# Optimization experiments

Measured on AMD Instinct MI355X. Metric: run time of the kernel, lower is better.

## Reference

```python
import jax, jax.numpy as jnp
import numpy as np

B, C, H, W = 2, 3, 512, 512
P = 16
D = 768
NH = 12
DEPTH = 12
MLP = 4
HP, WP = H // P, W // P
N = HP * WP
DH = D // NH          # 64
ROPE_BASE = 100.0     # from pos_embed='RoPE100'


def _ln(x, w, b, eps):
    m = jnp.mean(x, -1, keepdims=True)
    v = jnp.mean((x - m) ** 2, -1, keepdims=True)
    return (x - m) * jax.lax.rsqrt(v + eps) * w + b


def _rope_tables(maxpos, d):
    inv = 1.0 / (ROPE_BASE ** (jnp.arange(0, d, 2, dtype=jnp.float32) / d))
    f = jnp.arange(maxpos, dtype=jnp.float32)[:, None] * inv[None, :]
    f = jnp.concatenate([f, f], -1)  # [maxpos, d]
    return jnp.cos(f), jnp.sin(f)


def _rot_half(x):
    x1, x2 = jnp.split(x, 2, -1)
    return jnp.concatenate([-x2, x1], -1)


def _rope2d(t, pos, cos, sin):
    # t: [B,NH,N,DH]; pos: [B,N,2] (y,x). First half of DH rotated by y, second by x.
    def rot1d(tok, p):
        c = cos[p][:, None]  # [B,1,N,DH//2]
        s = sin[p][:, None]
        return tok * c + _rot_half(tok) * s
    ty, tx = jnp.split(t, 2, -1)
    return jnp.concatenate([rot1d(ty, pos[..., 0]), rot1d(tx, pos[..., 1])], -1)


def _forward(image, patch_w, patch_b, ln1_w, ln1_b, qkv_w, qkv_b, proj_w, proj_b,
             ln2_w, ln2_b, fc1_w, fc1_b, fc2_w, fc2_b, encn_w, encn_b):
    # patch embed: conv stride=patch, flatten row-major (y-major, matching cartesian_prod(y,x))
    x = jax.lax.conv_general_dilated(image, patch_w, (P, P), 'VALID',
                                     dimension_numbers=('NCHW', 'OIHW', 'NCHW'))
    x = (x + patch_b[None, :, None, None]).reshape(B, D, N).transpose(0, 2, 1)  # [B,N,D]
    yy, xx = jnp.meshgrid(jnp.arange(HP), jnp.arange(WP), indexing='ij')
    pos = jnp.broadcast_to(jnp.stack([yy, xx], -1).reshape(N, 2), (B, N, 2))
    cos, sin = _rope_tables(max(HP, WP), DH // 2)
    scale = DH ** -0.5
    for i in range(DEPTH):
        h = _ln(x, ln1_w[i], ln1_b[i], 1e-5)
        qkv = (h @ qkv_w[i].T + qkv_b[i]).reshape(B, N, 3, NH, DH).transpose(2, 0, 3, 1, 4)
        q, k, v = qkv[0], qkv[1], qkv[2]  # [B,NH,N,DH]
        q = _rope2d(q, pos, cos, sin)
        k = _rope2d(k, pos, cos, sin)
        att = jax.nn.softmax(jnp.einsum('bhqd,bhkd->bhqk', q, k) * scale, -1)
        o = jnp.einsum('bhqk,bhkd->bhqd', att, v).transpose(0, 2, 1, 3).reshape(B, N, D)
        x = x + o @ proj_w[i].T + proj_b[i]
        h = _ln(x, ln2_w[i], ln2_b[i], 1e-5)
        h = jax.nn.gelu(h @ fc1_w[i].T + fc1_b[i], approximate=False)
        x = x + h @ fc2_w[i].T + fc2_b[i]
    x = _ln(x, encn_w, encn_b, 1e-6)
    return x, pos


def setup_inputs() -> dict:
    key = jax.random.key(0)
    ks = jax.random.split(key, 8)
    s = 0.02
    dff = MLP * D
    return {
        "image": jax.random.normal(ks[0], (B, C, H, W), jnp.float32),
        "true_shape": jnp.full((B, 2), H, jnp.int32),
        "patch_w": jax.random.normal(ks[1], (D, C, P, P), jnp.float32) * s,
        "patch_b": jnp.zeros((D,), jnp.float32),
        "ln1_w": jnp.ones((DEPTH, D), jnp.float32),
        "ln1_b": jnp.zeros((DEPTH, D), jnp.float32),
        "qkv_w": jax.random.normal(ks[2], (DEPTH, 3 * D, D), jnp.float32) * s,
        "qkv_b": jnp.zeros((DEPTH, 3 * D), jnp.float32),
        "proj_w": jax.random.normal(ks[3], (DEPTH, D, D), jnp.float32) * s,
        "proj_b": jnp.zeros((DEPTH, D), jnp.float32),
        "ln2_w": jnp.ones((DEPTH, D), jnp.float32),
        "ln2_b": jnp.zeros((DEPTH, D), jnp.float32),
        "fc1_w": jax.random.normal(ks[4], (DEPTH, dff, D), jnp.float32) * s,
        "fc1_b": jnp.zeros((DEPTH, dff), jnp.float32),
        "fc2_w": jax.random.normal(ks[5], (DEPTH, D, dff), jnp.float32) * s,
        "fc2_b": jnp.zeros((DEPTH, D), jnp.float32),
        "encn_w": jnp.ones((D,), jnp.float32),
        "encn_b": jnp.zeros((D,), jnp.float32),
    }


def reference(image, true_shape, patch_w, patch_b, ln1_w, ln1_b, qkv_w, qkv_b,
              proj_w, proj_b, ln2_w, ln2_b, fc1_w, fc1_b, fc2_w, fc2_b,
              encn_w, encn_b):
    # true_shape assumed full-resolution (all images H x W); positions are static grid
    return _forward(image, patch_w, patch_b, ln1_w, ln1_b, qkv_w, qkv_b, proj_w,
                    proj_b, ln2_w, ln2_b, fc1_w, fc1_b, fc2_w, fc2_b, encn_w, encn_b)
```

## Files before the change

kernel.cpp:

```cpp
#include <hip/hip_runtime.h>
#include <hip/hip_bf16.h>
#include <stdint.h>

typedef unsigned short u16;
typedef __attribute__((ext_vector_type(8))) short bf16x8;
typedef __attribute__((ext_vector_type(4))) float f32x4;
typedef __attribute__((ext_vector_type(4))) u16 u16x4;
typedef __attribute__((ext_vector_type(4))) uint32_t u32x4;

__device__ __forceinline__ u16 f2bf(float f) {
  union { float f; uint32_t u; } v; v.f = f;
  uint32_t u = v.u + 0x7FFFu + ((v.u >> 16) & 1u);
  return (u16)(u >> 16);
}
__device__ __forceinline__ float bf2f(u16 h) {
  union { uint32_t u; float f; } v; v.u = ((uint32_t)h) << 16;
  return v.f;
}

__device__ __forceinline__ int xcd_swz(int hw, int n) {
  return (n & 7) ? hw : (hw & 7) * (n >> 3) + (hw >> 3);
}

__device__ __forceinline__ void gload_lds16(const void* g, void* l) {
  __builtin_amdgcn_global_load_lds(
      (const __attribute__((address_space(1))) void*)g,
      (__attribute__((address_space(3))) void*)l, 16, 0, 0);
}

__global__ __launch_bounds__(256) void cast_f32_bf16(const float* __restrict__ src,
                                                     u16* __restrict__ dst, int n4) {
  int i = blockIdx.x * 256 + threadIdx.x;
  if (i < n4) {
    float4 v = ((const float4*)src)[i];
    u16x4 o; o.x = f2bf(v.x); o.y = f2bf(v.y); o.z = f2bf(v.z); o.w = f2bf(v.w);
    ((u16x4*)dst)[i] = o;
  }
}

__global__ __launch_bounds__(256) void im2col_kernel(const float* __restrict__ img,
                                                     u16* __restrict__ out) {
  int f = blockIdx.x * 256 + threadIdx.x;
  int row = blockIdx.y;
  int b = row >> 10, n = row & 1023, py = n >> 5, px = n & 31;
  int c = f >> 8, rem = f & 255, i = rem >> 4, j = rem & 15;
  float v = img[(((size_t)b * 3 + c) * 512 + py * 16 + i) * 512 + px * 16 + j];
  out[(size_t)row * 768 + f] = f2bf(v);
}

template <int EPI>
__global__ __launch_bounds__(256, 2)
void gemm_bt(const u16* __restrict__ A, const u16* __restrict__ W,
             const float* __restrict__ bias, void* __restrict__ outp,
             int M, int N, int K, int lda, int ldw) {
  constexpr int AB = 128 * 128;
  constexpr int BB = 128 * 128;
  constexpr int BUF = AB + BB;
  constexpr int LOADS = BUF / 4096;
  __shared__ char smem[2 * BUF];
  const int tid = threadIdx.x;
  const int lane = tid & 63;
  const int w = tid >> 6;
  const int qr = lane & 15;
  const int kg = lane >> 4;
  const int gx = gridDim.x;
  const int lid = xcd_swz(blockIdx.x + blockIdx.y * gx, gx * gridDim.y);
  const int bn = lid % gx, bm = lid / gx;
  const int wr = (w >> 1) * 64;
  const int wc = (w & 1) * 64;
  const size_t arow0 = (size_t)bm * 128;
  const size_t wrow0 = (size_t)bn * 128;
  const u16* Ab = A + (size_t)blockIdx.z * K;
  const u16* Wb = W + (size_t)blockIdx.z * K;

  f32x4 acc[4][4] = {};

  auto stage = [&](int buf, int kt) {
    char* As = smem + buf * BUF;
    char* Ws = As + AB;
#pragma unroll
    for (int r = 0; r < 4; ++r) {
      int o = r * 4096 + tid * 16;
      int row = o >> 7;
      int lc = (o & 127) ^ ((row & 7) << 4);
      gload_lds16(Ab + (arow0 + row) * lda + kt + (lc >> 1), As + o);
    }
#pragma unroll
    for (int r = 0; r < 4; ++r) {
      int o = r * 4096 + tid * 16;
      int row = o >> 7;
      int lc = (o & 127) ^ ((row & 7) << 4);
      gload_lds16(Wb + (wrow0 + row) * ldw + kt + (lc >> 1), Ws + o);
    }
  };

  const int nt = K >> 6;
  stage(0, 0);
  stage(1, 64);
  for (int t = 0; t < nt; ++t) {
    if (t + 1 < nt) {
      asm volatile("s_waitcnt vmcnt(%0)" :: "i"(LOADS) : "memory");
    } else {
      asm volatile("s_waitcnt vmcnt(0)" ::: "memory");
    }
    __builtin_amdgcn_s_barrier();
    const char* As = smem + (t & 1) * BUF;
    const char* Ws = As + AB;
    bf16x8 af[2][4], bfr[2][4];
#pragma unroll
    for (int m = 0; m < 4; ++m) {
      int row = wr + m * 16 + qr;
      af[0][m] = *(const bf16x8*)(As + row * 128 + ((kg * 16) ^ ((row & 7) << 4)));
    }
#pragma unroll
    for (int n = 0; n < 4; ++n) {
      int row = wc + n * 16 + qr;
      bfr[0][n] = *(const bf16x8*)(Ws + row * 128 + ((kg * 16) ^ ((row & 7) << 4)));
    }
    __builtin_amdgcn_sched_barrier(0);
#pragma unroll
    for (int m = 0; m < 4; ++m) {
      int row = wr + m * 16 + qr;
      af[1][m] = *(const bf16x8*)(As + row * 128 + ((64 + kg * 16) ^ ((row & 7) << 4)));
    }
#pragma unroll
    for (int n = 0; n < 4; ++n) {
      int row = wc + n * 16 + qr;
      bfr[1][n] = *(const bf16x8*)(Ws + row * 128 + ((64 + kg * 16) ^ ((row & 7) << 4)));
    }
    asm volatile("s_waitcnt lgkmcnt(8)" ::: "memory");
    __builtin_amdgcn_sched_barrier(0);
#pragma unroll
    for (int m = 0; m < 4; ++m)
#pragma unroll
      for (int n = 0; n < 4; ++n)
        acc[m][n] = __builtin_amdgcn_mfma_f32_16x16x32_bf16(af[0][m], bfr[0][n], acc[m][n], 0, 0, 0);
    asm volatile("s_waitcnt lgkmcnt(0)" ::: "memory");
    __builtin_amdgcn_sched_barrier(0);
    __builtin_amdgcn_s_barrier();
    if (t + 2 < nt) stage(t & 1, (t + 2) << 6);
#pragma unroll
    for (int m = 0; m < 4; ++m)
#pragma unroll
      for (int n = 0; n < 4; ++n)
        acc[m][n] = __builtin_amdgcn_mfma_f32_16x16x32_bf16(af[1][m], bfr[1][n], acc[m][n], 0, 0, 0);
  }

  const int r0 = bm * 128 + wr + kg * 4;
  const int c0 = bn * 128 + wc + qr;
  if constexpr (EPI == 4) {
    const int headbase = bn * 128 + wc;
    const bool isqk = headbase < 1536;
    const float linv = exp2f(-0.41524101186092122f * (float)qr);
    u16* outb = (u16*)outp;
#pragma unroll
    for (int m = 0; m < 4; ++m) {
#pragma unroll
      for (int j = 0; j < 4; ++j) {
        int row = r0 + m * 16 + j;
        int tok = row & 1023;
        float vs[4];
#pragma unroll
        for (int n = 0; n < 4; ++n) vs[n] = acc[m][n][j] + bias[c0 + n * 16];
        if (isqk) {
          float sy, cy, sx, cx;
          __sincosf((float)(tok >> 5) * linv, &sy, &cy);
          __sincosf((float)(tok & 31) * linv, &sx, &cx);
          float a0 = vs[0], a1 = vs[1], a2 = vs[2], a3 = vs[3];
          vs[0] = a0 * cy - a1 * sy;
          vs[1] = a1 * cy + a0 * sy;
          vs[2] = a2 * cx - a3 * sx;
          vs[3] = a3 * cx + a2 * sx;
        }
#pragma unroll
        for (int n = 0; n < 4; ++n)
          outb[(size_t)row * N + c0 + n * 16] = f2bf(vs[n]);
      }
    }
  } else if constexpr (EPI == 5) {
    u16* outb = (u16*)outp + (size_t)blockIdx.z * M * N;
#pragma unroll
    for (int m = 0; m < 4; ++m)
#pragma unroll
      for (int j = 0; j < 4; ++j) {
        int row = r0 + m * 16 + j;
#pragma unroll
        for (int n = 0; n < 4; ++n)
          outb[(size_t)row * N + c0 + n * 16] = f2bf(acc[m][n][j]);
      }
  } else {
    u16* outb = (u16*)outp;
#pragma unroll
    for (int m = 0; m < 4; ++m)
#pragma unroll
      for (int j = 0; j < 4; ++j) {
        int row = r0 + m * 16 + j;
#pragma unroll
        for (int n = 0; n < 4; ++n) {
          int col = c0 + n * 16;
          float v = acc[m][n][j] + bias[col];
          v = 0.5f * v * (1.0f + erff(v * 0.70710678118654752f));
          outb[(size_t)row * N + col] = f2bf(v);
        }
      }
  }
}

template <int FINAL>
__global__ __launch_bounds__(192)
void fuse_red_ln(const u16* __restrict__ parts, const float* __restrict__ bias,
                 const float* __restrict__ resid, float* __restrict__ xout,
                 void* __restrict__ lnout, const float* __restrict__ lw,
                 const float* __restrict__ lb, float eps) {
  if (FINAL && blockIdx.x >= 2048) {
    int i = (blockIdx.x - 2048) * 192 + threadIdx.x;
    if (i < 4096) {
      int c = i & 1, n = (i >> 1) & 1023;
      ((float*)lnout)[(size_t)2048 * 768 + i] = (float)(c ? (n & 31) : (n >> 5));
    }
    return;
  }
  const int row = blockIdx.x, t = threadIdx.x;
  const int c0 = t * 4;
  constexpr size_t MN = (size_t)2048 * 768;
  const u16x4 pa = *(const u16x4*)(parts + (size_t)row * 768 + c0);
  const u16x4 pb = *(const u16x4*)(parts + MN + (size_t)row * 768 + c0);
  const f32x4 bi = *(const f32x4*)(bias + c0);
  f32x4 v;
#pragma unroll
  for (int j = 0; j < 4; ++j) v[j] = bf2f(pa[j]) + bf2f(pb[j]) + bi[j];
  if (resid) v += *(const f32x4*)(resid + (size_t)row * 768 + c0);
  *(f32x4*)(xout + (size_t)row * 768 + c0) = v;
  float s = (v[0] + v[1]) + (v[2] + v[3]);
  float sq = (v[0] * v[0] + v[1] * v[1]) + (v[2] * v[2] + v[3] * v[3]);
#pragma unroll
  for (int m = 1; m < 64; m <<= 1) {
    s += __shfl_xor(s, m);
    sq += __shfl_xor(sq, m);
  }
  __shared__ float red[6];
  int wv = t >> 6;
  if ((t & 63) == 0) { red[wv] = s; red[3 + wv] = sq; }
  __syncthreads();
  s = red[0] + red[1] + red[2];
  sq = red[3] + red[4] + red[5];
  float mean = s * (1.0f / 768.0f);
  float var = sq * (1.0f / 768.0f) - mean * mean;
  float rstd = rsqrtf(var + eps);
  const f32x4 lwv = *(const f32x4*)(lw + c0);
  const f32x4 lbv = *(const f32x4*)(lb + c0);
  if (FINAL) {
    f32x4 o;
#pragma unroll
    for (int j = 0; j < 4; ++j) o[j] = (v[j] - mean) * rstd * lwv[j] + lbv[j];
    *(f32x4*)((float*)lnout + (size_t)row * 768 + c0) = o;
  } else {
    u16x4 o;
#pragma unroll
    for (int j = 0; j < 4; ++j) o[j] = f2bf((v[j] - mean) * rstd * lwv[j] + lbv[j]);
    *(u16x4*)((u16*)lnout + (size_t)row * 768 + c0) = o;
  }
}

__global__ __launch_bounds__(256)
void attn_kernel(const u16* __restrict__ qkv, u16* __restrict__ o) {
  __shared__ char smem[32768];
  const int tid = threadIdx.x, lane = tid & 63, w = tid >> 6;
  const int qr = lane & 15, kg = lane >> 4;
  const bool kgodd = (kg & 1) != 0;
  const int lid = xcd_swz(blockIdx.x, gridDim.x);
  const int qb = lid & 15, bh = lid >> 4;
  const int b = bh / 12, h = bh % 12;
  const int qrow0 = qb * 64 + w * 16;
  const u16* kvb = qkv + (size_t)b * 1024 * 2304;

  bf16x8 aq[2];
  {
    const u16* qbase = qkv + ((size_t)(b * 1024 + qrow0 + qr)) * 2304 + h * 64;
    aq[0] = *(const bf16x8*)(qbase + kg * 8);
    aq[1] = *(const bf16x8*)(qbase + 32 + kg * 8);
#pragma unroll
    for (int r = 0; r < 2; ++r)
#pragma unroll
      for (int e = 0; e < 8; ++e)
        aq[r][e] = (short)f2bf(bf2f((u16)aq[r][e]) * 0.125f);
  }
  f32x4 oacc[4] = {};
  float lsum = 0.f;

  const int kvp = tid >> 3, dg = tid & 7;
  bf16x8 va, vb;
  auto issueV = [&](int kt) {
    const u16* vsrc = kvb + ((size_t)(kt * 64 + kvp * 2)) * 2304 + 1536 + h * 64 + dg * 8;
    va = *(const bf16x8*)vsrc;
    vb = *(const bf16x8*)(vsrc + 2304);
  };
  auto issueK = [&](int kt, int bsel) {
    char* Ks = smem + bsel * 8192;
#pragma unroll
    for (int r = 0; r < 2; ++r) {
      int off = r * 4096 + tid * 16;
      int kv = off >> 7;
      int db = (off ^ ((kv & 7) << 4)) & 127;
      gload_lds16(kvb + ((size_t)(kt * 64 + kv)) * 2304 + 768 + h * 64 + (db >> 1), Ks + off);
    }
  };
  auto writeV = [&](int bsel) {
    char* Vt = smem + 16384 + bsel * 8192;
#pragma unroll
    for (int j = 0; j < 8; ++j) {
      int d = dg * 8 + j;
      uint32_t pk = (uint32_t)(u16)va[j] | ((uint32_t)(u16)vb[j] << 16);
      *(uint32_t*)(Vt + ((d * 128 + kvp * 4) ^ (((dg ^ j) & 7) << 4))) = pk;
    }
  };

  issueV(0);
  issueK(0, 0);
  writeV(0);

  for (int kt = 0; kt < 16; ++kt) {
    const int c = kt & 1;
    asm volatile("s_waitcnt vmcnt(0) lgkmcnt(0)" ::: "memory");
    __builtin_amdgcn_s_barrier();
    if (kt + 1 < 16) { issueV(kt + 1); issueK(kt + 1, c ^ 1); }

    const char* Ks = smem + c * 8192;
    const char* Vt = smem + 16384 + c * 8192;

    bf16x8 bk[2][4];
#pragma unroll
    for (int n = 0; n < 4; ++n) {
      int row = n * 16 + qr;
      bk[0][n] = *(const bf16x8*)(Ks + ((row * 128 + kg * 16) ^ ((row & 7) << 4)));
    }
    __builtin_amdgcn_sched_barrier(0);
#pragma unroll
    for (int n = 0; n < 4; ++n) {
      int row = n * 16 + qr;
      bk[1][n] = *(const bf16x8*)(Ks + ((row * 128 + 64 + kg * 16) ^ ((row & 7) << 4)));
    }
    f32x4 sa[4] = {};
    asm volatile("s_waitcnt lgkmcnt(4)" ::: "memory");
    __builtin_amdgcn_sched_barrier(0);
    __builtin_amdgcn_s_setprio(1);
#pragma unroll
    for (int n = 0; n < 4; ++n)
      sa[n] = __builtin_amdgcn_mfma_f32_16x16x32_bf16(bk[0][n], aq[0], sa[n], 0, 0, 0);
    asm volatile("s_waitcnt lgkmcnt(0)" ::: "memory");
    __builtin_amdgcn_sched_barrier(0);
#pragma unroll
    for (int n = 0; n < 4; ++n)
      sa[n] = __builtin_amdgcn_mfma_f32_16x16x32_bf16(bk[1][n], aq[1], sa[n], 0, 0, 0);
    __builtin_amdgcn_s_setprio(0);

    float pv[4][4];
    float ts = 0.f;
#pragma unroll
    for (int n = 0; n < 4; ++n)
#pragma unroll
      for (int j = 0; j < 4; ++j) {
        pv[n][j] = __expf(sa[n][j]);
        ts += pv[n][j];
      }
    lsum += ts;

    if (kt + 1 < 16) writeV(c ^ 1);

    bf16x8 vf[2][4];
#pragma unroll
    for (int ks = 0; ks < 2; ++ks)
#pragma unroll
      for (int n = 0; n < 4; ++n) {
        int d = n * 16 + qr;
        vf[ks][n] = *(const bf16x8*)(Vt + ((d * 128 + ks * 64 + kg * 16) ^ ((((d >> 3) ^ (d & 7)) & 7) << 4)));
      }

    uint32_t pk0[4], pk1[4];
#pragma unroll
    for (int n = 0; n < 4; ++n) {
      asm("v_cvt_pk_bf16_f32 %0, %1, %2" : "=v"(pk0[n]) : "v"(pv[n][0]), "v"(pv[n][1]));
      asm("v_cvt_pk_bf16_f32 %0, %1, %2" : "=v"(pk1[n]) : "v"(pv[n][2]), "v"(pv[n][3]));
    }
    bf16x8 pb[2];
#pragma unroll
    for (int ks = 0; ks < 2; ++ks) {
      uint32_t A0 = pk0[ks * 2], B0 = pk0[ks * 2 + 1];
      uint32_t A1 = pk1[ks * 2], B1 = pk1[ks * 2 + 1];
      asm("v_permlane32_swap_b32 %0, %1" : "+v"(A0), "+v"(B0));
      asm("v_permlane32_swap_b32 %0, %1" : "+v"(A1), "+v"(B1));
      uint32_t sA0 = (uint32_t)__shfl_xor((int)A0, 16);
      uint32_t sA1 = (uint32_t)__shfl_xor((int)A1, 16);
      uint32_t sB0 = (uint32_t)__shfl_xor((int)B0, 16);
      uint32_t sB1 = (uint32_t)__shfl_xor((int)B1, 16);
      u32x4 dd;
      dd.x = kgodd ? sB0 : A0;
      dd.y = kgodd ? sB1 : A1;
      dd.z = kgodd ? B0 : sA0;
      dd.w = kgodd ? B1 : sA1;
      pb[ks] = __builtin_bit_cast(bf16x8, dd);
    }

    __builtin_amdgcn_s_setprio(1);
#pragma unroll
    for (int ks = 0; ks < 2; ++ks)
#pragma unroll
      for (int n = 0; n < 4; ++n)
        oacc[n] = __builtin_amdgcn_mfma_f32_16x16x32_bf16(vf[ks][n], pb[ks], oacc[n], 0, 0, 0);
    __builtin_amdgcn_s_setprio(0);
  }
  lsum += __shfl_xor(lsum, 16);
  lsum += __shfl_xor(lsum, 32);
  float inv = 1.0f / lsum;
  const size_t rowg = (size_t)(b * 1024 + qrow0 + qr);
#pragma unroll
  for (int n = 0; n < 4; ++n) {
    u16x4 ov;
#pragma unroll
    for (int j = 0; j < 4; ++j) ov[j] = f2bf(oacc[n][j] * inv);
    *(u16x4*)(o + rowg * 768 + h * 64 + n * 16 + kg * 4) = ov;
  }
}

extern "C" void kernel_launch(void* const* d_in, const int* in_sizes, int n_in,
                              void* d_out, int out_size, void* d_ws, size_t ws_size,
                              hipStream_t stream) {
  const float* image  = (const float*)d_in[0];
  const float* patch_w = (const float*)d_in[2];
  const float* patch_b = (const float*)d_in[3];
  const float* ln1_w = (const float*)d_in[4];
  const float* ln1_b = (const float*)d_in[5];
  const float* qkv_w = (const float*)d_in[6];
  const float* qkv_b = (const float*)d_in[7];
  const float* proj_w = (const float*)d_in[8];
  const float* proj_b = (const float*)d_in[9];
  const float* ln2_w = (const float*)d_in[10];
  const float* ln2_b = (const float*)d_in[11];
  const float* fc1_w = (const float*)d_in[12];
  const float* fc1_b = (const float*)d_in[13];
  const float* fc2_w = (const float*)d_in[14];
  const float* fc2_b = (const float*)d_in[15];
  const float* encn_w = (const float*)d_in[16];
  const float* encn_b = (const float*)d_in[17];

  char* ws = (char*)d_ws;
  size_t off = 0;
  auto alloc = [&](size_t bytes) {
    char* pr = ws + off;
    off += (bytes + 255) & ~(size_t)255;
    return pr;
  };

  float* x    = (float*)alloc((size_t)2048 * 768 * 4);
  u16* hbuf   = (u16*)alloc((size_t)2048 * 768 * 2);
  u16* qkvb   = (u16*)alloc((size_t)2048 * 2304 * 2);
  u16* obuf   = (u16*)alloc((size_t)2048 * 768 * 2);
  u16* h2     = (u16*)alloc((size_t)2048 * 3072 * 2);
  u16* wpb    = (u16*)alloc((size_t)768 * 768 * 2);
  u16* parts  = (u16*)alloc((size_t)2 * 2048 * 768 * 2);

  const size_t wq_n = (size_t)12 * 2304 * 768;
  const size_t wp_n = (size_t)12 * 768 * 768;
  const size_t w1_n = (size_t)12 * 3072 * 768;
  const size_t w2_n = (size_t)12 * 3072 * 768;
  bool upfront = (off + 2 * (wq_n + wp_n + w1_n + w2_n) + (1u << 20)) <= ws_size;

  u16 *wq, *wp, *w1, *w2;
  if (upfront) {
    wq = (u16*)alloc(wq_n * 2);
    wp = (u16*)alloc(wp_n * 2);
    w1 = (u16*)alloc(w1_n * 2);
    w2 = (u16*)alloc(w2_n * 2);
  } else {
    wq = (u16*)alloc((size_t)2304 * 768 * 2);
    wp = (u16*)alloc((size_t)768 * 768 * 2);
    w1 = (u16*)alloc((size_t)3072 * 768 * 2);
    w2 = (u16*)alloc((size_t)3072 * 768 * 2);
  }

  auto cast = [&](const float* s, u16* d, size_t n) {
    int n4 = (int)(n / 4);
    cast_f32_bf16<<<(n4 + 255) / 256, 256, 0, stream>>>(s, d, n4);
  };

  cast(patch_w, wpb, (size_t)768 * 768);
  if (upfront) {
    cast(qkv_w, wq, wq_n);
    cast(proj_w, wp, wp_n);
    cast(fc1_w, w1, w1_n);
    cast(fc2_w, w2, w2_n);
  }

  im2col_kernel<<<dim3(3, 2048), 256, 0, stream>>>(image, hbuf);
  gemm_bt<5><<<dim3(6, 16, 2), 256, 0, stream>>>(hbuf, wpb, nullptr, parts, 2048, 768, 384, 768, 768);
  fuse_red_ln<0><<<2048, 192, 0, stream>>>(parts, patch_b, nullptr, x, hbuf, ln1_w, ln1_b, 1e-5f);

  for (int L = 0; L < 12; ++L) {
    u16 *wqL, *wpL, *w1L, *w2L;
    if (upfront) {
      wqL = wq + (size_t)L * 2304 * 768;
      wpL = wp + (size_t)L * 768 * 768;
      w1L = w1 + (size_t)L * 3072 * 768;
      w2L = w2 + (size_t)L * 3072 * 768;
    } else {
      cast(qkv_w + (size_t)L * 2304 * 768, wq, (size_t)2304 * 768);
      cast(proj_w + (size_t)L * 768 * 768, wp, (size_t)768 * 768);
      cast(fc1_w + (size_t)L * 3072 * 768, w1, (size_t)3072 * 768);
      cast(fc2_w + (size_t)L * 768 * 3072, w2, (size_t)3072 * 768);
      wqL = wq; wpL = wp; w1L = w1; w2L = w2;
    }
    gemm_bt<4><<<dim3(18, 16), 256, 0, stream>>>(hbuf, wqL, qkv_b + L * 2304, qkvb, 2048, 2304, 768, 768, 768);
    attn_kernel<<<384, 256, 0, stream>>>(qkvb, obuf);
    gemm_bt<5><<<dim3(6, 16, 2), 256, 0, stream>>>(obuf, wpL, nullptr, parts, 2048, 768, 384, 768, 768);
    fuse_red_ln<0><<<2048, 192, 0, stream>>>(parts, proj_b + L * 768, x, x, hbuf,
                                             ln2_w + L * 768, ln2_b + L * 768, 1e-5f);
    gemm_bt<1><<<dim3(24, 16), 256, 0, stream>>>(hbuf, w1L, fc1_b + L * 3072, h2, 2048, 3072, 768, 768, 768);
    gemm_bt<5><<<dim3(6, 16, 2), 256, 0, stream>>>(h2, w2L, nullptr, parts, 2048, 768, 1536, 3072, 3072);
    if (L < 11) {
      fuse_red_ln<0><<<2048, 192, 0, stream>>>(parts, fc2_b + L * 768, x, x, hbuf,
                                               ln1_w + (L + 1) * 768, ln1_b + (L + 1) * 768, 1e-5f);
    } else {
      fuse_red_ln<1><<<2070, 192, 0, stream>>>(parts, fc2_b + L * 768, x, x, (float*)d_out,
                                               encn_w, encn_b, 1e-6f);
    }
  }
}
```

Baseline: 1.281 ms.

## Add XCD-aware GEMM tile mapping, bf16 residual stream, and smaller attention blocks

GEMM blocks are now remapped so that each of the 8 XCDs gets a contiguous sub-grid of output tiles, including the split-K z dimension, to improve L2 reuse of A and W tiles. The residual stream x is stored as bf16 instead of fp32, which halves its read and write traffic in the fused reduce+LayerNorm kernels but adds rounding error on every residual add. Attention blocks are cut to 128 threads covering 32 query rows, doubling the block count, with K and V staging loops adjusted to match.

```diff
diff --git a/kernel.cpp b/kernel.cpp
--- a/kernel.cpp
+++ b/kernel.cpp
@@ -48,7 +48,7 @@
   out[(size_t)row * 768 + f] = f2bf(v);
 }
 
-template <int EPI>
+template <int EPI, int XGX, int XGY, int XGZ>
 __global__ __launch_bounds__(256, 2)
 void gemm_bt(const u16* __restrict__ A, const u16* __restrict__ W,
              const float* __restrict__ bias, void* __restrict__ outp,
@@ -63,15 +63,21 @@
   const int w = tid >> 6;
   const int qr = lane & 15;
   const int kg = lane >> 4;
-  const int gx = gridDim.x;
-  const int lid = xcd_swz(blockIdx.x + blockIdx.y * gx, gx * gridDim.y);
-  const int bn = lid % gx, bm = lid / gx;
+  const int gx = gridDim.x, gy = gridDim.y;
+  const int hw = blockIdx.x + gx * (blockIdx.y + gy * blockIdx.z);
+  const int xcd = hw & 7, i = hw >> 3;
+  const int sx = gx / XGX, sy = gy / XGY;
+  const int cx = xcd % XGX, cy = (xcd / XGX) % XGY, cz = xcd / (XGX * XGY);
+  const int bn = cx * sx + i % sx;
+  const int rr_ = i / sx;
+  const int bm = cy * sy + rr_ % sy;
+  const int bz = cz * (gridDim.z / XGZ) + rr_ / sy;
   const int wr = (w >> 1) * 64;
   const int wc = (w & 1) * 64;
   const size_t arow0 = (size_t)bm * 128;
   const size_t wrow0 = (size_t)bn * 128;
-  const u16* Ab = A + (size_t)blockIdx.z * K;
-  const u16* Wb = W + (size_t)blockIdx.z * K;
+  const u16* Ab = A + (size_t)bz * K;
+  const u16* Wb = W + (size_t)bz * K;
 
   f32x4 acc[4][4] = {};
 
@@ -163,14 +169,14 @@
 #pragma unroll
         for (int n = 0; n < 4; ++n) vs[n] = acc[m][n][j] + bias[c0 + n * 16];
         if (isqk) {
-          float sy, cy, sx, cx;
+          float sy, cy, sxv, cxv;
           __sincosf((float)(tok >> 5) * linv, &sy, &cy);
-          __sincosf((float)(tok & 31) * linv, &sx, &cx);
+          __sincosf((float)(tok & 31) * linv, &sxv, &cxv);
           float a0 = vs[0], a1 = vs[1], a2 = vs[2], a3 = vs[3];
           vs[0] = a0 * cy - a1 * sy;
           vs[1] = a1 * cy + a0 * sy;
-          vs[2] = a2 * cx - a3 * sx;
-          vs[3] = a3 * cx + a2 * sx;
+          vs[2] = a2 * cxv - a3 * sxv;
+          vs[3] = a3 * cxv + a2 * sxv;
         }
 #pragma unroll
         for (int n = 0; n < 4; ++n)
@@ -178,7 +184,7 @@
       }
     }
   } else if constexpr (EPI == 5) {
-    u16* outb = (u16*)outp + (size_t)blockIdx.z * M * N;
+    u16* outb = (u16*)outp + (size_t)bz * M * N;
 #pragma unroll
     for (int m = 0; m < 4; ++m)
 #pragma unroll
@@ -209,7 +215,7 @@
 template <int FINAL>
 __global__ __launch_bounds__(192)
 void fuse_red_ln(const u16* __restrict__ parts, const float* __restrict__ bias,
-                 const float* __restrict__ resid, float* __restrict__ xout,
+                 const u16* __restrict__ resid, u16* __restrict__ xout,
                  void* __restrict__ lnout, const float* __restrict__ lw,
                  const float* __restrict__ lb, float eps) {
   if (FINAL && blockIdx.x >= 2048) {
@@ -229,8 +235,19 @@
   f32x4 v;
 #pragma unroll
   for (int j = 0; j < 4; ++j) v[j] = bf2f(pa[j]) + bf2f(pb[j]) + bi[j];
-  if (resid) v += *(const f32x4*)(resid + (size_t)row * 768 + c0);
-  *(f32x4*)(xout + (size_t)row * 768 + c0) = v;
+  if (resid) {
+    const u16x4 rv = *(const u16x4*)(resid + (size_t)row * 768 + c0);
+#pragma unroll
+    for (int j = 0; j < 4; ++j) v[j] += bf2f(rv[j]);
+  }
+  if (xout) {
+    u16x4 xo;
+#pragma unroll
+    for (int j = 0; j < 4; ++j) xo[j] = f2bf(v[j]);
+    *(u16x4*)(xout + (size_t)row * 768 + c0) = xo;
+#pragma unroll
+    for (int j = 0; j < 4; ++j) v[j] = bf2f(xo[j]);
+  }
   float s = (v[0] + v[1]) + (v[2] + v[3]);
   float sq = (v[0] * v[0] + v[1] * v[1]) + (v[2] * v[2] + v[3] * v[3]);
 #pragma unroll
@@ -262,16 +279,16 @@
   }
 }
 
-__global__ __launch_bounds__(256)
+__global__ __launch_bounds__(128)
 void attn_kernel(const u16* __restrict__ qkv, u16* __restrict__ o) {
   __shared__ char smem[32768];
   const int tid = threadIdx.x, lane = tid & 63, w = tid >> 6;
   const int qr = lane & 15, kg = lane >> 4;
   const bool kgodd = (kg & 1) != 0;
   const int lid = xcd_swz(blockIdx.x, gridDim.x);
-  const int qb = lid & 15, bh = lid >> 4;
+  const int qb = lid & 31, bh = lid >> 5;
   const int b = bh / 12, h = bh % 12;
-  const int qrow0 = qb * 64 + w * 16;
+  const int qrow0 = qb * 32 + w * 16;
   const u16* kvb = qkv + (size_t)b * 1024 * 2304;
 
   bf16x8 aq[2];
@@ -289,17 +306,21 @@
   float lsum = 0.f;
 
   const int kvp = tid >> 3, dg = tid & 7;
-  bf16x8 va, vb;
+  bf16x8 va[2], vb[2];
   auto issueV = [&](int kt) {
-    const u16* vsrc = kvb + ((size_t)(kt * 64 + kvp * 2)) * 2304 + 1536 + h * 64 + dg * 8;
-    va = *(const bf16x8*)vsrc;
-    vb = *(const bf16x8*)(vsrc + 2304);
+#pragma unroll
+    for (int rr = 0; rr < 2; ++rr) {
+      int p = rr * 16 + kvp;
+      const u16* vsrc = kvb + ((size_t)(kt * 64 + 2 * p)) * 2304 + 1536 + h * 64 + dg * 8;
+      va[rr] = *(const bf16x8*)vsrc;
+      vb[rr] = *(const bf16x8*)(vsrc + 2304);
+    }
   };
   auto issueK = [&](int kt, int bsel) {
     char* Ks = smem + bsel * 8192;
 #pragma unroll
-    for (int r = 0; r < 2; ++r) {
-      int off = r * 4096 + tid * 16;
+    for (int r = 0; r < 4; ++r) {
+      int off = r * 2048 + tid * 16;
       int kv = off >> 7;
       int db = (off ^ ((kv & 7) << 4)) & 127;
       gload_lds16(kvb + ((size_t)(kt * 64 + kv)) * 2304 + 768 + h * 64 + (db >> 1), Ks + off);
@@ -308,10 +329,14 @@
   auto writeV = [&](int bsel) {
     char* Vt = smem + 16384 + bsel * 8192;
 #pragma unroll
-    for (int j = 0; j < 8; ++j) {
-      int d = dg * 8 + j;
-      uint32_t pk = (uint32_t)(u16)va[j] | ((uint32_t)(u16)vb[j] << 16);
-      *(uint32_t*)(Vt + ((d * 128 + kvp * 4) ^ (((dg ^ j) & 7) << 4))) = pk;
+    for (int rr = 0; rr < 2; ++rr) {
+      int p = rr * 16 + kvp;
+#pragma unroll
+      for (int j = 0; j < 8; ++j) {
+        int d = dg * 8 + j;
+        uint32_t pk = (uint32_t)(u16)va[rr][j] | ((uint32_t)(u16)vb[rr][j] << 16);
+        *(uint32_t*)(Vt + ((d * 128 + p * 4) ^ (((dg ^ j) & 7) << 4))) = pk;
+      }
     }
   };
 
@@ -451,7 +476,7 @@
     return pr;
   };
 
-  float* x    = (float*)alloc((size_t)2048 * 768 * 4);
+  u16* x      = (u16*)alloc((size_t)2048 * 768 * 2);
   u16* hbuf   = (u16*)alloc((size_t)2048 * 768 * 2);
   u16* qkvb   = (u16*)alloc((size_t)2048 * 2304 * 2);
   u16* obuf   = (u16*)alloc((size_t)2048 * 768 * 2);
@@ -492,7 +517,7 @@
   }
 
   im2col_kernel<<<dim3(3, 2048), 256, 0, stream>>>(image, hbuf);
-  gemm_bt<5><<<dim3(6, 16, 2), 256, 0, stream>>>(hbuf, wpb, nullptr, parts, 2048, 768, 384, 768, 768);
+  gemm_bt<5, 2, 2, 2><<<dim3(6, 16, 2), 256, 0, stream>>>(hbuf, wpb, nullptr, parts, 2048, 768, 384, 768, 768);
   fuse_red_ln<0><<<2048, 192, 0, stream>>>(parts, patch_b, nullptr, x, hbuf, ln1_w, ln1_b, 1e-5f);
 
   for (int L = 0; L < 12; ++L) {
@@ -509,18 +534,18 @@
       cast(fc2_w + (size_t)L * 768 * 3072, w2, (size_t)3072 * 768);
       wqL = wq; wpL = wp; w1L = w1; w2L = w2;
     }
-    gemm_bt<4><<<dim3(18, 16), 256, 0, stream>>>(hbuf, wqL, qkv_b + L * 2304, qkvb, 2048, 2304, 768, 768, 768);
-    attn_kernel<<<384, 256, 0, stream>>>(qkvb, obuf);
-    gemm_bt<5><<<dim3(6, 16, 2), 256, 0, stream>>>(obuf, wpL, nullptr, parts, 2048, 768, 384, 768, 768);
+    gemm_bt<4, 2, 4, 1><<<dim3(18, 16), 256, 0, stream>>>(hbuf, wqL, qkv_b + L * 2304, qkvb, 2048, 2304, 768, 768, 768);
+    attn_kernel<<<768, 128, 0, stream>>>(qkvb, obuf);
+    gemm_bt<5, 2, 2, 2><<<dim3(6, 16, 2), 256, 0, stream>>>(obuf, wpL, nullptr, parts, 2048, 768, 384, 768, 768);
     fuse_red_ln<0><<<2048, 192, 0, stream>>>(parts, proj_b + L * 768, x, x, hbuf,
                                              ln2_w + L * 768, ln2_b + L * 768, 1e-5f);
-    gemm_bt<1><<<dim3(24, 16), 256, 0, stream>>>(hbuf, w1L, fc1_b + L * 3072, h2, 2048, 3072, 768, 768, 768);
-    gemm_bt<5><<<dim3(6, 16, 2), 256, 0, stream>>>(h2, w2L, nullptr, parts, 2048, 768, 1536, 3072, 3072);
+    gemm_bt<1, 2, 4, 1><<<dim3(24, 16), 256, 0, stream>>>(hbuf, w1L, fc1_b + L * 3072, h2, 2048, 3072, 768, 768, 768);
+    gemm_bt<5, 2, 2, 2><<<dim3(6, 16, 2), 256, 0, stream>>>(h2, w2L, nullptr, parts, 2048, 768, 1536, 3072, 3072);
     if (L < 11) {
       fuse_red_ln<0><<<2048, 192, 0, stream>>>(parts, fc2_b + L * 768, x, x, hbuf,
                                                ln1_w + (L + 1) * 768, ln1_b + (L + 1) * 768, 1e-5f);
     } else {
-      fuse_red_ln<1><<<2070, 192, 0, stream>>>(parts, fc2_b + L * 768, x, x, (float*)d_out,
+      fuse_red_ln<1><<<2070, 192, 0, stream>>>(parts, fc2_b + L * 768, x, nullptr, (float*)d_out,
                                                encn_w, encn_b, 1e-6f);
     }
   }
```

Result: faster. 1.245 ms (-2.8%).
